# Performance work log

Hardware: AMD Instinct MI355X
Metric: run time of the kernel (lower is better)

Reference implementation:

```python
import jax, jax.numpy as jnp
import numpy as np
import math

B, N, Q, K = 1, 64, 512, 512
C_Q = C_K = C_V = 256
C_HIDDEN = 32
NO_HEADS = 8
HID = C_HIDDEN * NO_HEADS  # 256


def setup_inputs() -> dict:
    key = jax.random.key(0)
    ks = jax.random.split(key, 12)
    inp = {
        "q_x": jax.random.normal(ks[0], (B, N, Q, C_Q), jnp.float32),
        "k_x": jax.random.normal(ks[1], (B, N, K, C_K), jnp.float32),
        "v_x": jax.random.normal(ks[2], (B, N, K, C_V), jnp.float32),
        "bias_mask": jax.random.normal(ks[3], (B, N, 1, 1, K), jnp.float32),
        "bias_pair": jax.random.normal(ks[4], (B, 1, NO_HEADS, Q, K), jnp.float32),
        # projection weights stored [in, out] (torch Linear is [out, in])
        "wq": jax.random.normal(ks[5], (C_Q, HID), jnp.float32) / math.sqrt(C_Q),
        "wk": jax.random.normal(ks[6], (C_K, HID), jnp.float32) / math.sqrt(C_K),
        "wv": jax.random.normal(ks[7], (C_V, HID), jnp.float32) / math.sqrt(C_V),
        # gating: init weights=0, bias=1 in the module; use small random for a non-trivial test
        "wg": jax.random.normal(ks[8], (C_Q, HID), jnp.float32) * 0.02,
        "bg": jnp.ones((HID,), jnp.float32),
        # output: init 'final' (zeros); use small random for a non-trivial test
        "wo": jax.random.normal(ks[9], (HID, C_Q), jnp.float32) * 0.02,
        "bo": jnp.zeros((C_Q,), jnp.float32),
    }
    return inp


def reference(q_x, k_x, v_x, bias_mask, bias_pair, wq, wk, wv, wg, bg, wo, bo):
    h, c = NO_HEADS, C_HIDDEN
    # projections -> [B, N, Q/K, H, C_h]
    q = (q_x @ wq).reshape(*q_x.shape[:-1], h, c) / math.sqrt(c)
    k = (k_x @ wk).reshape(*k_x.shape[:-1], h, c)
    v = (v_x @ wv).reshape(*v_x.shape[:-1], h, c)
    # logits [B, N, H, Q, K] with additive biases
    a = jnp.einsum("bnqhc,bnkhc->bnhqk", q, k) + bias_mask + bias_pair
    a = jax.nn.softmax(a, axis=-1)
    # output [B, N, Q, H, C_h]
    o = jnp.einsum("bnhqk,bnkhc->bnqhc", a, v)
    # gating
    g = jax.nn.sigmoid((q_x @ wg + bg).reshape(*q_x.shape[:-1], h, c))
    o = o * g
    o = o.reshape(*o.shape[:-2], h * c)
    return o @ wo + bo
```

## Files before the change

kernel.cpp:

```cpp
#include <hip/hip_runtime.h>
#include <math.h>

#define NSEQ   64
#define QLEN   512
#define KLEN   512
#define CIN    256
#define HEADS  8
#define CH     32
#define HIDDIM 256
#define M_TOTAL (NSEQ * QLEN)
#define L2E    1.4426950408889634f

typedef _Float16 f16x8 __attribute__((ext_vector_type(8)));
typedef _Float16 f16x4 __attribute__((ext_vector_type(4)));
typedef __fp16   fp16x2 __attribute__((ext_vector_type(2)));
typedef float    f32x4 __attribute__((ext_vector_type(4)));

__device__ __forceinline__ void gload16(const void* g, void* l) {
    __builtin_amdgcn_global_load_lds(
        (const __attribute__((address_space(1))) void*)g,
        (__attribute__((address_space(3))) void*)l, 16, 0, 0);
}

__device__ __forceinline__ float exp2_fast(float x) {
#if __has_builtin(__builtin_amdgcn_exp2f)
    return __builtin_amdgcn_exp2f(x);
#else
    float r; asm("v_exp_f32 %0, %1" : "=v"(r) : "v"(x)); return r;
#endif
}

__global__ __launch_bounds__(256) void wcast_kernel(
    const float* __restrict__ w0, const float* __restrict__ w1,
    const float* __restrict__ w2, const float* __restrict__ w3,
    const float* __restrict__ w4, _Float16* __restrict__ wt)
{
    __shared__ float t[64][65];
    const float* W;
    switch (blockIdx.z) {
        case 0: W = w0; break; case 1: W = w1; break;
        case 2: W = w2; break; case 3: W = w3; break;
        default: W = w4;
    }
    _Float16* WT = wt + (size_t)blockIdx.z * 65536;
    const int i0 = blockIdx.x * 64, o0 = blockIdx.y * 64;
    const int tid = threadIdx.x;
    const int rr = tid >> 4, c4 = tid & 15;
    #pragma unroll
    for (int i = 0; i < 4; ++i) {
        const int row = rr + i * 16;
        *(float4*)&t[row][c4 * 4] = *(const float4*)&W[(size_t)(i0 + row) * 256 + o0 + c4 * 4];
    }
    __syncthreads();
    #pragma unroll
    for (int i = 0; i < 4; ++i) {
        const int row = rr + i * 16;
        f16x4 v;
        #pragma unroll
        for (int j = 0; j < 4; ++j) v[j] = (_Float16)t[c4 * 4 + j][row];
        *(f16x4*)&WT[(size_t)(o0 + row) * 256 + i0 + c4 * 4] = v;
    }
}

__global__ __launch_bounds__(256) void bpfrag_kernel(
    const float* __restrict__ bias_pair, float* __restrict__ frag)
{
    __shared__ float t[64][68];
    const int qb = blockIdx.x, kb = blockIdx.y, h = blockIdx.z;
    const int tid = threadIdx.x;
    #pragma unroll
    for (int i = 0; i < 4; ++i) {
        const int idx = tid + i * 256;
        const int r = idx >> 4, c4 = idx & 15;
        *(float4*)&t[r][c4 * 4] = *(const float4*)
            &bias_pair[((size_t)h * QLEN + qb * 64 + r) * KLEN + kb * 64 + c4 * 4];
    }
    __syncthreads();
    const int lane = tid & 63, w = tid >> 6;
    const int l15 = lane & 15, quad = lane >> 4;
    const int qt = qb * 4 + w;
    #pragma unroll
    for (int kt2 = 0; kt2 < 4; ++kt2) {
        const int kt = kb * 4 + kt2;
        float4 v;
        v.x = (t[w * 16 + l15][kt2 * 16 + quad * 4 + 0] - 4.0f) * L2E;
        v.y = (t[w * 16 + l15][kt2 * 16 + quad * 4 + 1] - 4.0f) * L2E;
        v.z = (t[w * 16 + l15][kt2 * 16 + quad * 4 + 2] - 4.0f) * L2E;
        v.w = (t[w * 16 + l15][kt2 * 16 + quad * 4 + 3] - 4.0f) * L2E;
        *(float4*)&frag[(((size_t)(h * 32 + qt) * 32) + kt) * 256 + lane * 4] = v;
    }
}

__global__ __launch_bounds__(256) void bmscale_kernel(
    const float* __restrict__ bm, float* __restrict__ o)
{
    const int i = blockIdx.x * 256 + threadIdx.x;
    float4 v = *(const float4*)(bm + (size_t)i * 4);
    v.x *= L2E; v.y *= L2E; v.z *= L2E; v.w *= L2E;
    *(float4*)(o + (size_t)i * 4) = v;
}

__global__ __launch_bounds__(256, 3) void proj_gemm_kernel(
    const float* __restrict__ q_x, const float* __restrict__ k_x,
    const float* __restrict__ v_x, const _Float16* __restrict__ wT,
    const float* __restrict__ bg,
    _Float16* __restrict__ oq, _Float16* __restrict__ ok,
    _Float16* __restrict__ ovT, _Float16* __restrict__ og)
{
    __shared__ __attribute__((aligned(16))) _Float16 A_s[2][32 * 256];

    const int combo = blockIdx.x >> 7;
    const int blk   = blockIdx.x & 127;
    const int mode  = combo >> 1;
    const int nhalf = combo & 1;
    const float* A = (mode <= 1) ? q_x : (mode == 2) ? k_x : v_x;
    const _Float16* BT = wT + (size_t)mode * 65536;

    const int tid  = threadIdx.x;
    const int lane = tid & 63, w = tid >> 6;
    const int l15  = lane & 15, quad = lane >> 4;
    const int nw   = nhalf * 128 + w * 32;

    f16x8 bfr[2][8];
    #pragma unroll
    for (int nt = 0; nt < 2; ++nt)
        #pragma unroll
        for (int ks = 0; ks < 8; ++ks)
            bfr[nt][ks] = *(const f16x8*)(BT +
                (size_t)(nw + nt * 16 + l15) * 256 + ks * 32 + quad * 8);

    float4 bg4[2] = {{0.f,0.f,0.f,0.f},{0.f,0.f,0.f,0.f}};
    if (mode == 1) {
        bg4[0] = *(const float4*)&bg[nw + quad * 4];
        bg4[1] = *(const float4*)&bg[nw + 16 + quad * 4];
    }

    const int row_base = blk * 256;

    f32x4 acc[2][2];
    #pragma unroll
    for (int mt = 0; mt < 2; ++mt)
        #pragma unroll
        for (int nt = 0; nt < 2; ++nt) acc[mt][nt] = (f32x4){0.f, 0.f, 0.f, 0.f};

    float4 sreg[8];

    auto gload_panel = [&](int panel) {
        const int row0 = row_base + panel * 32;
        #pragma unroll
        for (int j = 0; j < 4; ++j) {
            const int p = tid + j * 256;
            const int r = p >> 5, c = p & 31;
            const float* ap = A + (size_t)(row0 + r) * 256 + c * 8;
            sreg[j * 2]     = *(const float4*)ap;
            sreg[j * 2 + 1] = *(const float4*)(ap + 4);
        }
    };

    auto swrite_panel = [&](int buf) {
        #pragma unroll
        for (int j = 0; j < 4; ++j) {
            const int p = tid + j * 256;
            const int r = p >> 5, c = p & 31;
            const int cp = c ^ (r & 15);
            f16x8 v;
            v[0] = (_Float16)sreg[j * 2].x;     v[1] = (_Float16)sreg[j * 2].y;
            v[2] = (_Float16)sreg[j * 2].z;     v[3] = (_Float16)sreg[j * 2].w;
            v[4] = (_Float16)sreg[j * 2 + 1].x; v[5] = (_Float16)sreg[j * 2 + 1].y;
            v[6] = (_Float16)sreg[j * 2 + 1].z; v[7] = (_Float16)sreg[j * 2 + 1].w;
            *(f16x8*)&A_s[buf][(r * 32 + cp) * 8] = v;
        }
    };

    gload_panel(0);
    swrite_panel(0);
    __syncthreads();

    for (int i = 0; i < 8; ++i) {
        const int buf = i & 1;
        if (i < 7) gload_panel(i + 1);

        #pragma unroll
        for (int ks = 0; ks < 8; ++ks) {
            f16x8 af[2];
            #pragma unroll
            for (int mt = 0; mt < 2; ++mt) {
                const int r  = mt * 16 + l15;
                const int cp = (ks * 4 + quad) ^ (r & 15);
                af[mt] = *(const f16x8*)&A_s[buf][(r * 32 + cp) * 8];
            }
            if (mode != 3) {
                #pragma unroll
                for (int mt = 0; mt < 2; ++mt)
                    #pragma unroll
                    for (int nt = 0; nt < 2; ++nt)
                        acc[mt][nt] = __builtin_amdgcn_mfma_f32_16x16x32_f16(
                            bfr[nt][ks], af[mt], acc[mt][nt], 0, 0, 0);
            } else {
                #pragma unroll
                for (int mt = 0; mt < 2; ++mt)
                    #pragma unroll
                    for (int nt = 0; nt < 2; ++nt)
                        acc[mt][nt] = __builtin_amdgcn_mfma_f32_16x16x32_f16(
                            af[mt], bfr[nt][ks], acc[mt][nt], 0, 0, 0);
            }
        }

        const int row0 = row_base + i * 32;
        if (mode == 3) {
            #pragma unroll
            for (int mt = 0; mt < 2; ++mt) {
                #pragma unroll
                for (int nt = 0; nt < 2; ++nt) {
                    const int col  = nw + nt * 16 + l15;
                    const int rowg = row0 + mt * 16 + quad * 4;
                    const int nn = rowg >> 9, kpos = rowg & 511;
                    f16x4 st;
                    #pragma unroll
                    for (int reg = 0; reg < 4; ++reg) st[reg] = (_Float16)acc[mt][nt][reg];
                    *(f16x4*)&ovT[((size_t)(nn * 256 + col)) * 512 + kpos] = st;
                }
            }
        } else {
            _Float16* C = (mode == 0) ? oq : (mode == 1) ? og : ok;
            #pragma unroll
            for (int mt = 0; mt < 2; ++mt) {
                const int mrow = row0 + mt * 16 + l15;
                #pragma unroll
                for (int nt = 0; nt < 2; ++nt) {
                    const int colb = nw + nt * 16 + quad * 4;
                    f16x4 st;
                    #pragma unroll
                    for (int reg = 0; reg < 4; ++reg) {
                        float x = acc[mt][nt][reg];
                        if (mode == 0) x *= 0.2550348614f;
                        if (mode == 1) {
                            x += ((const float*)&bg4[nt])[reg];
                            x = 1.0f / (1.0f + __expf(-x));
                        }
                        st[reg] = (_Float16)x;
                    }
                    *(f16x4*)&C[(size_t)mrow * HIDDIM + colb] = st;
                }
            }
        }
        #pragma unroll
        for (int mt = 0; mt < 2; ++mt)
            #pragma unroll
            for (int nt = 0; nt < 2; ++nt) acc[mt][nt] = (f32x4){0.f, 0.f, 0.f, 0.f};

        if (i < 7) swrite_panel(buf ^ 1);
        __syncthreads();
    }
}

__global__ __launch_bounds__(256, 3) void outproj_kernel(
    const _Float16* __restrict__ Ain, const _Float16* __restrict__ BT,
    const float* __restrict__ bias, float* __restrict__ Cout)
{
    __shared__ __attribute__((aligned(16))) _Float16 A_s[2][32 * 256];

    const int blk   = blockIdx.x & 511;
    const int nhalf = blockIdx.x >> 9;
    const int tid  = threadIdx.x;
    const int lane = tid & 63, w = tid >> 6;
    const int l15  = lane & 15, quad = lane >> 4;
    const int nw   = nhalf * 128 + w * 32;

    f16x8 bfr[2][8];
    #pragma unroll
    for (int nt = 0; nt < 2; ++nt)
        #pragma unroll
        for (int ks = 0; ks < 8; ++ks)
            bfr[nt][ks] = *(const f16x8*)(BT +
                (size_t)(nw + nt * 16 + l15) * 256 + ks * 32 + quad * 8);

    const float4 bias4[2] = {
        *(const float4*)&bias[nw + quad * 4],
        *(const float4*)&bias[nw + 16 + quad * 4],
    };
    const int row_base = blk * 64;

    f32x4 acc[2][2];
    #pragma unroll
    for (int mt = 0; mt < 2; ++mt)
        #pragma unroll
        for (int nt = 0; nt < 2; ++nt) acc[mt][nt] = (f32x4){0.f, 0.f, 0.f, 0.f};

    auto stage = [&](int panel, int buf) {
        const int row0 = row_base + panel * 32;
        #pragma unroll
        for (int j = 0; j < 4; ++j) {
            const int p = tid + j * 256;
            const int r = p >> 5, c = p & 31;
            const int cl = (c & ~7) | ((c & 7) ^ (r & 7));
            gload16(Ain + (size_t)(row0 + r) * 256 + cl * 8, &A_s[buf][p * 8]);
        }
    };

    stage(0, 0);
    __syncthreads();

    for (int i = 0; i < 2; ++i) {
        if (i < 1) stage(i + 1, (i + 1) & 1);
        const int buf = i & 1;

        #pragma unroll
        for (int ks = 0; ks < 8; ++ks) {
            f16x8 af[2];
            #pragma unroll
            for (int mt = 0; mt < 2; ++mt) {
                const int r = mt * 16 + l15;
                const int c = (ks * 4 + quad) ^ (r & 7);
                af[mt] = *(const f16x8*)&A_s[buf][r * 256 + c * 8];
            }
            #pragma unroll
            for (int mt = 0; mt < 2; ++mt)
                #pragma unroll
                for (int nt = 0; nt < 2; ++nt)
                    acc[mt][nt] = __builtin_amdgcn_mfma_f32_16x16x32_f16(
                        bfr[nt][ks], af[mt], acc[mt][nt], 0, 0, 0);
        }

        const int row0 = row_base + i * 32;
        #pragma unroll
        for (int mt = 0; mt < 2; ++mt) {
            const int mrow = row0 + mt * 16 + l15;
            #pragma unroll
            for (int nt = 0; nt < 2; ++nt) {
                const int colb = nw + nt * 16 + quad * 4;
                float4 st;
                st.x = acc[mt][nt][0] + bias4[nt].x;
                st.y = acc[mt][nt][1] + bias4[nt].y;
                st.z = acc[mt][nt][2] + bias4[nt].z;
                st.w = acc[mt][nt][3] + bias4[nt].w;
                *(float4*)&Cout[(size_t)mrow * HIDDIM + colb] = st;
            }
        }
        #pragma unroll
        for (int mt = 0; mt < 2; ++mt)
            #pragma unroll
            for (int nt = 0; nt < 2; ++nt) acc[mt][nt] = (f32x4){0.f, 0.f, 0.f, 0.f};

        __syncthreads();
    }
}

__global__ __launch_bounds__(256, 4) void attn_kernel(
    const _Float16* __restrict__ qb, const _Float16* __restrict__ kb,
    const _Float16* __restrict__ vT, const _Float16* __restrict__ gb,
    _Float16* __restrict__ ob,
    const float* __restrict__ bm2, const float* __restrict__ bp_frag)
{
    __shared__ _Float16 k_s[128][40];
    __shared__ _Float16 v_s[32][136];

    const int n    = blockIdx.x;
    const int h    = blockIdx.y;
    const int q0   = blockIdx.z * 128;
    const int tid  = threadIdx.x;
    const int lane = tid & 63;
    const int wq   = tid >> 6;
    const int l15  = lane & 15;
    const int quad = lane >> 4;

    f16x8 qf[2];
    #pragma unroll
    for (int qt = 0; qt < 2; ++qt)
        qf[qt] = *(const f16x8*)(qb +
            (size_t)(n * QLEN + q0 + wq * 32 + qt * 16 + l15) * HIDDIM + h * CH + quad * 8);

    const float* bpf = bp_frag +
        ((size_t)(h * 32 + blockIdx.z * 8 + wq * 2) * 32) * 256 + lane * 4;
    const float* bmb = bm2 + n * KLEN + quad * 4;

    f32x4 o_acc[2][2];
    float l_lane[2] = {0.f, 0.f};
    #pragma unroll
    for (int qt = 0; qt < 2; ++qt)
        #pragma unroll
        for (int ct = 0; ct < 2; ++ct) o_acc[qt][ct] = (f32x4){0.f, 0.f, 0.f, 0.f};

    for (int ch = 0; ch < 4; ++ch) {
        __syncthreads();
        #pragma unroll
        for (int i = 0; i < 2; ++i) {
            const int idx = tid + i * 256;
            const int r = idx >> 2, c8 = idx & 3;
            *(uint4*)&k_s[r][c8 * 8] = *(const uint4*)
                (kb + (size_t)(n * KLEN + ch * 128 + r) * HIDDIM + h * CH + c8 * 8);
            const int vr = idx >> 4, vs = idx & 15;
            *(uint4*)&v_s[vr][vs * 8] = *(const uint4*)
                (vT + ((size_t)(n * HEADS + h) * CH + vr) * KLEN + ch * 128 + vs * 8);
        }
        __syncthreads();

        #pragma unroll
        for (int kt = 0; kt < 8; ++kt) {
            const int kti = ch * 8 + kt;
            const f16x8 kf = *(const f16x8*)&k_s[kt * 16 + l15][quad * 8];
            const float4 bm  = *(const float4*)(bmb + ch * 128 + kt * 16);
            const float4 bp0 = *(const float4*)(bpf + (size_t)kti * 256);
            const float4 bp1 = *(const float4*)(bpf + (size_t)(32 + kti) * 256);
            f32x4 c0, c1;
            c0[0] = bm.x + bp0.x; c0[1] = bm.y + bp0.y;
            c0[2] = bm.z + bp0.z; c0[3] = bm.w + bp0.w;
            c1[0] = bm.x + bp1.x; c1[1] = bm.y + bp1.y;
            c1[2] = bm.z + bp1.z; c1[3] = bm.w + bp1.w;
            __builtin_amdgcn_s_setprio(1);
            const f32x4 s0 = __builtin_amdgcn_mfma_f32_16x16x32_f16(kf, qf[0], c0, 0, 0, 0);
            const f32x4 s1 = __builtin_amdgcn_mfma_f32_16x16x32_f16(kf, qf[1], c1, 0, 0, 0);
            __builtin_amdgcn_s_setprio(0);
            const f16x4 bv0 = *(const f16x4*)&v_s[l15][kt * 16 + quad * 4];
            const f16x4 bv1 = *(const f16x4*)&v_s[16 + l15][kt * 16 + quad * 4];
            #pragma unroll
            for (int qt = 0; qt < 2; ++qt) {
                const f32x4 s = qt ? s1 : s0;
                const float p0 = exp2_fast(s[0]);
                const float p1 = exp2_fast(s[1]);
                const float p2 = exp2_fast(s[2]);
                const float p3 = exp2_fast(s[3]);
                l_lane[qt] += (p0 + p1) + (p2 + p3);
                union { f16x4 v; fp16x2 h[2]; } u;
                u.h[0] = __builtin_amdgcn_cvt_pkrtz(p0, p1);
                u.h[1] = __builtin_amdgcn_cvt_pkrtz(p2, p3);
                __builtin_amdgcn_s_setprio(1);
                o_acc[qt][0] = __builtin_amdgcn_mfma_f32_16x16x16f16(u.v, bv0, o_acc[qt][0], 0, 0, 0);
                o_acc[qt][1] = __builtin_amdgcn_mfma_f32_16x16x16f16(u.v, bv1, o_acc[qt][1], 0, 0, 0);
                __builtin_amdgcn_s_setprio(0);
            }
        }
    }

    float invl[2][4];
    #pragma unroll
    for (int qt = 0; qt < 2; ++qt) {
        float lf = l_lane[qt];
        lf += __shfl_xor(lf, 16);
        lf += __shfl_xor(lf, 32);
        #pragma unroll
        for (int reg = 0; reg < 4; ++reg)
            invl[qt][reg] = 1.0f / __shfl(lf, quad * 4 + reg);
    }

    #pragma unroll
    for (int qt = 0; qt < 2; ++qt) {
        #pragma unroll
        for (int ct = 0; ct < 2; ++ct) {
            #pragma unroll
            for (int reg = 0; reg < 4; ++reg) {
                const int row = q0 + wq * 32 + qt * 16 + quad * 4 + reg;
                const size_t idx = (size_t)(n * QLEN + row) * HIDDIM + h * CH + ct * 16 + l15;
                const float g = (float)gb[idx];
                ob[idx] = (_Float16)(o_acc[qt][ct][reg] * invl[qt][reg] * g);
            }
        }
    }
}

extern "C" void kernel_launch(void* const* d_in, const int* in_sizes, int n_in,
                              void* d_out, int out_size, void* d_ws, size_t ws_size,
                              hipStream_t stream)
{
    const float* q_x       = (const float*)d_in[0];
    const float* k_x       = (const float*)d_in[1];
    const float* v_x       = (const float*)d_in[2];
    const float* bias_mask = (const float*)d_in[3];
    const float* bias_pair = (const float*)d_in[4];
    const float* wq        = (const float*)d_in[5];
    const float* wk        = (const float*)d_in[6];
    const float* wv        = (const float*)d_in[7];
    const float* wg        = (const float*)d_in[8];
    const float* bg        = (const float*)d_in[9];
    const float* wo        = (const float*)d_in[10];
    const float* bo        = (const float*)d_in[11];
    float* out = (float*)d_out;

    const size_t BUF = (size_t)M_TOTAL * HIDDIM;
    _Float16* ws_q  = (_Float16*)d_ws;
    _Float16* ws_k  = ws_q + BUF;
    _Float16* ws_vT = ws_k + BUF;
    _Float16* ws_g  = ws_vT + BUF;
    _Float16* ws_o  = ws_g + BUF;
    _Float16* wT    = ws_o + BUF;
    float*    bpf   = (float*)(wT + 5 * 65536);
    float*    bm2   = bpf + (size_t)8 * 512 * 512;

    wcast_kernel<<<dim3(4, 4, 5), 256, 0, stream>>>(wq, wg, wk, wv, wo, wT);
    bpfrag_kernel<<<dim3(8, 8, 8), 256, 0, stream>>>(bias_pair, bpf);
    bmscale_kernel<<<dim3(32), 256, 0, stream>>>(bias_mask, bm2);

    proj_gemm_kernel<<<dim3(1024), 256, 0, stream>>>(
        q_x, k_x, v_x, wT, bg, ws_q, ws_k, ws_vT, ws_g);

    attn_kernel<<<dim3(NSEQ, HEADS, QLEN / 128), 256, 0, stream>>>(
        ws_q, ws_k, ws_vT, ws_g, ws_o, bm2, bpf);

    outproj_kernel<<<dim3(1024), 256, 0, stream>>>(
        ws_o, wT + 4 * 65536, bo, out);
}
```

Baseline: 257.2 us.

## Deepen proj GEMM prefetch, preload outproj panels, fold bias-mask scaling into wcast

```diff
diff --git a/kernel.cpp b/kernel.cpp
--- a/kernel.cpp
+++ b/kernel.cpp
@@ -33,8 +33,19 @@
 __global__ __launch_bounds__(256) void wcast_kernel(
     const float* __restrict__ w0, const float* __restrict__ w1,
     const float* __restrict__ w2, const float* __restrict__ w3,
-    const float* __restrict__ w4, _Float16* __restrict__ wt)
+    const float* __restrict__ w4, const float* __restrict__ bm,
+    float* __restrict__ bm2, _Float16* __restrict__ wt)
 {
+    if (blockIdx.z == 5) {
+        const int id = ((blockIdx.y * 4 + blockIdx.x) * 256 + threadIdx.x) * 8;
+        float4 a = *(const float4*)(bm + id);
+        float4 b = *(const float4*)(bm + id + 4);
+        a.x *= L2E; a.y *= L2E; a.z *= L2E; a.w *= L2E;
+        b.x *= L2E; b.y *= L2E; b.z *= L2E; b.w *= L2E;
+        *(float4*)(bm2 + id) = a;
+        *(float4*)(bm2 + id + 4) = b;
+        return;
+    }
     __shared__ float t[64][65];
     const float* W;
     switch (blockIdx.z) {
@@ -91,15 +102,6 @@
     }
 }
 
-__global__ __launch_bounds__(256) void bmscale_kernel(
-    const float* __restrict__ bm, float* __restrict__ o)
-{
-    const int i = blockIdx.x * 256 + threadIdx.x;
-    float4 v = *(const float4*)(bm + (size_t)i * 4);
-    v.x *= L2E; v.y *= L2E; v.z *= L2E; v.w *= L2E;
-    *(float4*)(o + (size_t)i * 4) = v;
-}
-
 __global__ __launch_bounds__(256, 3) void proj_gemm_kernel(
     const float* __restrict__ q_x, const float* __restrict__ k_x,
     const float* __restrict__ v_x, const _Float16* __restrict__ wT,
@@ -143,43 +145,36 @@
         #pragma unroll
         for (int nt = 0; nt < 2; ++nt) acc[mt][nt] = (f32x4){0.f, 0.f, 0.f, 0.f};
 
-    float4 sreg[8];
-
-    auto gload_panel = [&](int panel) {
+    float4 sa[8], sb[8];
+
+    auto gloadP = [&](float4* s, int panel) {
         const int row0 = row_base + panel * 32;
         #pragma unroll
         for (int j = 0; j < 4; ++j) {
             const int p = tid + j * 256;
             const int r = p >> 5, c = p & 31;
             const float* ap = A + (size_t)(row0 + r) * 256 + c * 8;
-            sreg[j * 2]     = *(const float4*)ap;
-            sreg[j * 2 + 1] = *(const float4*)(ap + 4);
+            s[j * 2]     = *(const float4*)ap;
+            s[j * 2 + 1] = *(const float4*)(ap + 4);
         }
     };
 
-    auto swrite_panel = [&](int buf) {
+    auto swriteP = [&](const float4* s, int buf) {
         #pragma unroll
         for (int j = 0; j < 4; ++j) {
             const int p = tid + j * 256;
             const int r = p >> 5, c = p & 31;
             const int cp = c ^ (r & 15);
             f16x8 v;
-            v[0] = (_Float16)sreg[j * 2].x;     v[1] = (_Float16)sreg[j * 2].y;
-            v[2] = (_Float16)sreg[j * 2].z;     v[3] = (_Float16)sreg[j * 2].w;
-            v[4] = (_Float16)sreg[j * 2 + 1].x; v[5] = (_Float16)sreg[j * 2 + 1].y;
-            v[6] = (_Float16)sreg[j * 2 + 1].z; v[7] = (_Float16)sreg[j * 2 + 1].w;
+            v[0] = (_Float16)s[j * 2].x;     v[1] = (_Float16)s[j * 2].y;
+            v[2] = (_Float16)s[j * 2].z;     v[3] = (_Float16)s[j * 2].w;
+            v[4] = (_Float16)s[j * 2 + 1].x; v[5] = (_Float16)s[j * 2 + 1].y;
+            v[6] = (_Float16)s[j * 2 + 1].z; v[7] = (_Float16)s[j * 2 + 1].w;
             *(f16x8*)&A_s[buf][(r * 32 + cp) * 8] = v;
         }
     };
 
-    gload_panel(0);
-    swrite_panel(0);
-    __syncthreads();
-
-    for (int i = 0; i < 8; ++i) {
-        const int buf = i & 1;
-        if (i < 7) gload_panel(i + 1);
-
+    auto computeP = [&](int buf) {
         #pragma unroll
         for (int ks = 0; ks < 8; ++ks) {
             f16x8 af[2];
@@ -205,7 +200,9 @@
                             af[mt], bfr[nt][ks], acc[mt][nt], 0, 0, 0);
             }
         }
-
+    };
+
+    auto epilogueP = [&](int i) {
         const int row0 = row_base + i * 32;
         if (mode == 3) {
             #pragma unroll
@@ -248,13 +245,34 @@
         for (int mt = 0; mt < 2; ++mt)
             #pragma unroll
             for (int nt = 0; nt < 2; ++nt) acc[mt][nt] = (f32x4){0.f, 0.f, 0.f, 0.f};
-
-        if (i < 7) swrite_panel(buf ^ 1);
-        __syncthreads();
-    }
-}
-
-__global__ __launch_bounds__(256, 3) void outproj_kernel(
+    };
+
+    gloadP(sa, 0);
+    swriteP(sa, 0);
+    gloadP(sb, 1);
+    asm volatile("s_waitcnt lgkmcnt(0)" ::: "memory");
+    __builtin_amdgcn_s_barrier();
+
+    for (int ii = 0; ii < 4; ++ii) {
+        const int i0 = 2 * ii;
+        if (i0 + 2 < 8) gloadP(sa, i0 + 2);
+        computeP(0);
+        epilogueP(i0);
+        swriteP(sb, 1);
+        asm volatile("s_waitcnt lgkmcnt(0)" ::: "memory");
+        __builtin_amdgcn_s_barrier();
+        if (i0 + 3 < 8) gloadP(sb, i0 + 3);
+        computeP(1);
+        epilogueP(i0 + 1);
+        if (i0 + 2 < 8) {
+            swriteP(sa, 0);
+            asm volatile("s_waitcnt lgkmcnt(0)" ::: "memory");
+            __builtin_amdgcn_s_barrier();
+        }
+    }
+}
+
+__global__ __launch_bounds__(256, 4) void outproj_kernel(
     const _Float16* __restrict__ Ain, const _Float16* __restrict__ BT,
     const float* __restrict__ bias, float* __restrict__ Cout)
 {
@@ -266,6 +284,19 @@
     const int lane = tid & 63, w = tid >> 6;
     const int l15  = lane & 15, quad = lane >> 4;
     const int nw   = nhalf * 128 + w * 32;
+    const int row_base = blk * 64;
+
+    #pragma unroll
+    for (int pan = 0; pan < 2; ++pan) {
+        const int row0 = row_base + pan * 32;
+        #pragma unroll
+        for (int j = 0; j < 4; ++j) {
+            const int p = tid + j * 256;
+            const int r = p >> 5, c = p & 31;
+            const int cl = (c & ~7) | ((c & 7) ^ (r & 7));
+            gload16(Ain + (size_t)(row0 + r) * 256 + cl * 8, &A_s[pan][p * 8]);
+        }
+    }
 
     f16x8 bfr[2][8];
     #pragma unroll
@@ -279,31 +310,16 @@
         *(const float4*)&bias[nw + quad * 4],
         *(const float4*)&bias[nw + 16 + quad * 4],
     };
-    const int row_base = blk * 64;
-
-    f32x4 acc[2][2];
-    #pragma unroll
-    for (int mt = 0; mt < 2; ++mt)
-        #pragma unroll
-        for (int nt = 0; nt < 2; ++nt) acc[mt][nt] = (f32x4){0.f, 0.f, 0.f, 0.f};
-
-    auto stage = [&](int panel, int buf) {
-        const int row0 = row_base + panel * 32;
-        #pragma unroll
-        for (int j = 0; j < 4; ++j) {
-            const int p = tid + j * 256;
-            const int r = p >> 5, c = p & 31;
-            const int cl = (c & ~7) | ((c & 7) ^ (r & 7));
-            gload16(Ain + (size_t)(row0 + r) * 256 + cl * 8, &A_s[buf][p * 8]);
-        }
-    };
-
-    stage(0, 0);
+
     __syncthreads();
 
+    #pragma unroll
     for (int i = 0; i < 2; ++i) {
-        if (i < 1) stage(i + 1, (i + 1) & 1);
-        const int buf = i & 1;
+        f32x4 acc[2][2];
+        #pragma unroll
+        for (int mt = 0; mt < 2; ++mt)
+            #pragma unroll
+            for (int nt = 0; nt < 2; ++nt) acc[mt][nt] = (f32x4){0.f, 0.f, 0.f, 0.f};
 
         #pragma unroll
         for (int ks = 0; ks < 8; ++ks) {
@@ -312,7 +328,7 @@
             for (int mt = 0; mt < 2; ++mt) {
                 const int r = mt * 16 + l15;
                 const int c = (ks * 4 + quad) ^ (r & 7);
-                af[mt] = *(const f16x8*)&A_s[buf][r * 256 + c * 8];
+                af[mt] = *(const f16x8*)&A_s[i][r * 256 + c * 8];
             }
             #pragma unroll
             for (int mt = 0; mt < 2; ++mt)
@@ -337,12 +353,6 @@
                 *(float4*)&Cout[(size_t)mrow * HIDDIM + colb] = st;
             }
         }
-        #pragma unroll
-        for (int mt = 0; mt < 2; ++mt)
-            #pragma unroll
-            for (int nt = 0; nt < 2; ++nt) acc[mt][nt] = (f32x4){0.f, 0.f, 0.f, 0.f};
-
-        __syncthreads();
     }
 }
 
@@ -486,9 +496,9 @@
     float*    bpf   = (float*)(wT + 5 * 65536);
     float*    bm2   = bpf + (size_t)8 * 512 * 512;
 
-    wcast_kernel<<<dim3(4, 4, 5), 256, 0, stream>>>(wq, wg, wk, wv, wo, wT);
+    wcast_kernel<<<dim3(4, 4, 6), 256, 0, stream>>>(
+        wq, wg, wk, wv, wo, bias_mask, bm2, wT);
     bpfrag_kernel<<<dim3(8, 8, 8), 256, 0, stream>>>(bias_pair, bpf);
-    bmscale_kernel<<<dim3(32), 256, 0, stream>>>(bias_mask, bm2);
 
     proj_gemm_kernel<<<dim3(1024), 256, 0, stream>>>(
         q_x, k_x, v_x, wT, bg, ws_q, ws_k, ws_vT, ws_g);
```

New measurement: 328.7 us. +27.8%, slower.
